# Performance work log

Hardware: AMD Instinct MI355X
Metric: run time of the kernel (lower is better)

Reference implementation:

```python
import jax, jax.numpy as jnp
import numpy as np

N_HEADS = 8
D_KV = 64
NUM_BUCKETS = 32
MAX_DISTANCE = 128


def _relative_position_bucket(relative_position, bidirectional=True,
                              num_buckets=NUM_BUCKETS, max_distance=MAX_DISTANCE):
    # Faithful port of T5Attention._relative_position_bucket (bidirectional path).
    n = -relative_position
    if bidirectional:
        num_buckets //= 2
        ret = (n < 0).astype(jnp.int32) * num_buckets
        n = jnp.abs(n)
    else:
        ret = jnp.zeros_like(n)
        n = jnp.maximum(n, 0)
    max_exact = num_buckets // 2
    is_small = n < max_exact
    val_if_large = max_exact + (
        jnp.log(n.astype(jnp.float32) / max_exact)
        / np.log(max_distance / max_exact)
        * (num_buckets - max_exact)
    ).astype(jnp.int32)
    val_if_large = jnp.minimum(val_if_large, num_buckets - 1)
    return ret + jnp.where(is_small, n, val_if_large)


def setup_inputs() -> dict:
    key = jax.random.key(0)
    ks = jax.random.split(key, 6)
    bs, qlen, d_model = 2, 2048, 512
    inner = N_HEADS * D_KV
    s = 1.0 / np.sqrt(d_model)
    return {
        "input": jax.random.normal(ks[0], (bs, qlen, d_model), jnp.float32),
        "Wq": jax.random.normal(ks[1], (d_model, inner), jnp.float32) * s,
        "Wk": jax.random.normal(ks[2], (d_model, inner), jnp.float32) * s,
        "Wv": jax.random.normal(ks[3], (d_model, inner), jnp.float32) * s,
        "Wo": jax.random.normal(ks[4], (inner, d_model), jnp.float32) * s,
        "rel_bias": jax.random.normal(ks[5], (NUM_BUCKETS, N_HEADS), jnp.float32),
    }


def reference(input, Wq, Wk, Wv, Wo, rel_bias):
    bs, qlen, d_model = input.shape

    def shape(x):  # [b, s, inner] -> [b, h, s, d]
        return x.reshape(bs, qlen, N_HEADS, D_KV).transpose(0, 2, 1, 3)

    q = shape(input @ Wq)
    k = shape(input @ Wk)
    v = shape(input @ Wv)

    # Raw scores (T5: no 1/sqrt(d) scaling)
    scores = jnp.einsum("bhqd,bhkd->bhqk", q, k)

    # Relative position bias: bucket [q, k] -> [h, q, k]
    pos = jnp.arange(qlen)
    rel_pos = pos[None, :] - pos[:, None]  # memory - query
    buckets = _relative_position_bucket(rel_pos, bidirectional=True)
    position_bias = rel_bias[buckets].transpose(2, 0, 1)[None]  # [1, h, q, k]

    scores = scores + position_bias
    weights = jax.nn.softmax(scores.astype(jnp.float32), axis=-1).astype(scores.dtype)

    context = jnp.einsum("bhqk,bhkd->bhqd", weights, v)
    context = context.transpose(0, 2, 1, 3).reshape(bs, qlen, N_HEADS * D_KV)
    return context @ Wo
```

## Files before the change

kernel.cpp:

```cpp
#include <hip/hip_runtime.h>
#include <hip/hip_bf16.h>
#include <cmath>

typedef __bf16 bf16_t;
typedef __bf16 bf16x8 __attribute__((ext_vector_type(8)));
typedef __bf16 bf16x4 __attribute__((ext_vector_type(4)));
typedef float f32x4 __attribute__((ext_vector_type(4)));

#define QLEN 2048
#define DMODEL 512
#define NH 8
#define DKV 64
#define INNER 512
#define LOG2E 1.44269504f
#define THR_LOG2 11.5415603f

__global__ __launch_bounds__(256) void transpose512_split_all(
    const float* __restrict__ W0, const float* __restrict__ W1,
    const float* __restrict__ W2, const float* __restrict__ W3,
    bf16_t* __restrict__ H0, bf16_t* __restrict__ L0,
    bf16_t* __restrict__ H1, bf16_t* __restrict__ L1,
    bf16_t* __restrict__ H2, bf16_t* __restrict__ L2,
    bf16_t* __restrict__ H3, bf16_t* __restrict__ L3) {
  __shared__ float tile[32][33];
  int z = blockIdx.z;
  const float* W = z == 0 ? W0 : z == 1 ? W1 : z == 2 ? W2 : W3;
  bf16_t* Whi    = z == 0 ? H0 : z == 1 ? H1 : z == 2 ? H2 : H3;
  bf16_t* Wlo    = z == 0 ? L0 : z == 1 ? L1 : z == 2 ? L2 : L3;
  int bk = blockIdx.x * 32, bn = blockIdx.y * 32;
  int tx = threadIdx.x, ty = threadIdx.y;
  #pragma unroll
  for (int i = 0; i < 32; i += 8)
    tile[ty + i][tx] = W[(size_t)(bk + ty + i) * DMODEL + bn + tx];
  __syncthreads();
  #pragma unroll
  for (int i = 0; i < 32; i += 8) {
    float v = tile[tx][ty + i];
    bf16_t hb = (bf16_t)v;
    size_t o = (size_t)(bn + ty + i) * DMODEL + bk + tx;
    Whi[o] = hb;
    Wlo[o] = (bf16_t)(v - (float)hb);
  }
}

__device__ __forceinline__ void splitx8(const float4& v0, const float4& v1,
                                        bf16x8& h, bf16x8& l) {
  #pragma unroll
  for (int j = 0; j < 4; ++j) {
    float x = (&v0.x)[j];
    bf16_t hb = (bf16_t)x;
    h[j] = hb; l[j] = (bf16_t)(x - (float)hb);
  }
  #pragma unroll
  for (int j = 0; j < 4; ++j) {
    float x = (&v1.x)[j];
    bf16_t hb = (bf16_t)x;
    h[4 + j] = hb; l[4 + j] = (bf16_t)(x - (float)hb);
  }
}

#define GST 72

__global__ __launch_bounds__(256) void gemm_qkv(const float* __restrict__ X,
                                                const bf16_t* __restrict__ Wqh,
                                                const bf16_t* __restrict__ Wql,
                                                const bf16_t* __restrict__ Wkh,
                                                const bf16_t* __restrict__ Wkl,
                                                const bf16_t* __restrict__ Wvh,
                                                bf16_t* __restrict__ Qh,
                                                bf16_t* __restrict__ Ql,
                                                bf16_t* __restrict__ Kh,
                                                bf16_t* __restrict__ Vt) {
  __shared__ bf16_t sAh[64 * GST];
  __shared__ bf16_t sAl[64 * GST];
  __shared__ bf16_t sBh[128 * GST];
  __shared__ bf16_t sBl[128 * GST];
  const int m0 = blockIdx.x * 64;
  const int y = blockIdx.y;
  const int kind = y >> 2;
  const int n0 = (y & 3) * 128;
  const bf16_t* __restrict__ Bh = kind == 0 ? Wqh : kind == 1 ? Wkh : Wvh;
  const bf16_t* __restrict__ Bl = kind == 0 ? Wql : Wkl;

  const int tid = threadIdx.x;
  const int lane = tid & 63, w = tid >> 6;
  const int wr = (w >> 1) * 32, wc = (w & 1) * 64;
  const int l16 = lane & 15, lg = lane >> 4;

  f32x4 acc[2][4] = {};

  for (int k0 = 0; k0 < DMODEL; k0 += 64) {
    #pragma unroll
    for (int i = 0; i < 2; ++i) {
      int chunk = tid + i * 256;
      int row = chunk >> 3, c8 = (chunk & 7) * 8;
      const float4* src = reinterpret_cast<const float4*>(
          &X[(size_t)(m0 + row) * DMODEL + k0 + c8]);
      bf16x8 h, l;
      splitx8(src[0], src[1], h, l);
      *reinterpret_cast<bf16x8*>(&sAh[row * GST + c8]) = h;
      *reinterpret_cast<bf16x8*>(&sAl[row * GST + c8]) = l;
    }
    #pragma unroll
    for (int i = 0; i < 4; ++i) {
      int chunk = tid + i * 256;
      int row = chunk >> 3, c8 = (chunk & 7) * 8;
      size_t gb = (size_t)(n0 + row) * DMODEL + k0 + c8;
      *reinterpret_cast<bf16x8*>(&sBh[row * GST + c8]) = *reinterpret_cast<const bf16x8*>(&Bh[gb]);
      if (kind < 2)
        *reinterpret_cast<bf16x8*>(&sBl[row * GST + c8]) = *reinterpret_cast<const bf16x8*>(&Bl[gb]);
    }
    __syncthreads();
    #pragma unroll
    for (int ks = 0; ks < 2; ++ks) {
      bf16x8 ah[2], al[2], bh[4], bl[4];
      #pragma unroll
      for (int i = 0; i < 2; ++i) {
        int ro = (wr + i * 16 + l16) * GST + ks * 32 + lg * 8;
        ah[i] = *reinterpret_cast<const bf16x8*>(&sAh[ro]);
        al[i] = *reinterpret_cast<const bf16x8*>(&sAl[ro]);
      }
      #pragma unroll
      for (int j = 0; j < 4; ++j) {
        int ro = (wc + j * 16 + l16) * GST + ks * 32 + lg * 8;
        bh[j] = *reinterpret_cast<const bf16x8*>(&sBh[ro]);
        bl[j] = *reinterpret_cast<const bf16x8*>(&sBl[ro]);
      }
      #pragma unroll
      for (int i = 0; i < 2; ++i)
        #pragma unroll
        for (int j = 0; j < 4; ++j)
          acc[i][j] = __builtin_amdgcn_mfma_f32_16x16x32_bf16(ah[i], bh[j], acc[i][j], 0, 0, 0);
      if (kind < 2) {
        #pragma unroll
        for (int i = 0; i < 2; ++i)
          #pragma unroll
          for (int j = 0; j < 4; ++j) {
            acc[i][j] = __builtin_amdgcn_mfma_f32_16x16x32_bf16(ah[i], bl[j], acc[i][j], 0, 0, 0);
            acc[i][j] = __builtin_amdgcn_mfma_f32_16x16x32_bf16(al[i], bh[j], acc[i][j], 0, 0, 0);
          }
      }
    }
    __syncthreads();
  }

  #pragma unroll
  for (int i = 0; i < 2; ++i)
    #pragma unroll
    for (int j = 0; j < 4; ++j)
      #pragma unroll
      for (int r = 0; r < 4; ++r) {
        int m = m0 + wr + i * 16 + lg * 4 + r;
        int n = n0 + wc + j * 16 + l16;
        float v = acc[i][j][r];
        if (kind == 0) {
          v *= LOG2E;
          bf16_t hb = (bf16_t)v;
          size_t o = (size_t)m * INNER + n;
          Qh[o] = hb;
          Ql[o] = (bf16_t)(v - (float)hb);
        } else if (kind == 1) {
          Kh[(size_t)m * INNER + n] = (bf16_t)v;
        } else {
          int b = m >> 11, s = m & (QLEN - 1);
          Vt[(size_t)(b * INNER + n) * QLEN + s] = (bf16_t)v;
        }
      }
}

__global__ __launch_bounds__(256) void gemm_out(const bf16_t* __restrict__ A,
                                                const bf16_t* __restrict__ Bt,
                                                float* __restrict__ Cf) {
  __shared__ bf16_t sA[64 * GST];
  __shared__ bf16_t sB[64 * GST];
  const int m0 = blockIdx.x * 64, n0 = blockIdx.y * 64;
  const int tid = threadIdx.x;
  const int lane = tid & 63, w = tid >> 6;
  const int wr = (w >> 1) * 32, wc = (w & 1) * 32;
  const int l16 = lane & 15, lg = lane >> 4;

  f32x4 acc[2][2] = {};

  for (int k0 = 0; k0 < DMODEL; k0 += 64) {
    #pragma unroll
    for (int i = 0; i < 2; ++i) {
      int chunk = tid + i * 256;
      int row = chunk >> 3, c8 = (chunk & 7) * 8;
      *reinterpret_cast<bf16x8*>(&sA[row * GST + c8]) =
          *reinterpret_cast<const bf16x8*>(&A[(size_t)(m0 + row) * DMODEL + k0 + c8]);
      *reinterpret_cast<bf16x8*>(&sB[row * GST + c8]) =
          *reinterpret_cast<const bf16x8*>(&Bt[(size_t)(n0 + row) * DMODEL + k0 + c8]);
    }
    __syncthreads();
    #pragma unroll
    for (int ks = 0; ks < 2; ++ks) {
      bf16x8 af[2], bfr[2];
      #pragma unroll
      for (int i = 0; i < 2; ++i)
        af[i] = *reinterpret_cast<const bf16x8*>(&sA[(wr + i * 16 + l16) * GST + ks * 32 + lg * 8]);
      #pragma unroll
      for (int j = 0; j < 2; ++j)
        bfr[j] = *reinterpret_cast<const bf16x8*>(&sB[(wc + j * 16 + l16) * GST + ks * 32 + lg * 8]);
      #pragma unroll
      for (int i = 0; i < 2; ++i)
        #pragma unroll
        for (int j = 0; j < 2; ++j)
          acc[i][j] = __builtin_amdgcn_mfma_f32_16x16x32_bf16(af[i], bfr[j], acc[i][j], 0, 0, 0);
    }
    __syncthreads();
  }

  #pragma unroll
  for (int i = 0; i < 2; ++i)
    #pragma unroll
    for (int j = 0; j < 2; ++j)
      #pragma unroll
      for (int r = 0; r < 4; ++r) {
        int m = m0 + wr + i * 16 + lg * 4 + r;
        int n = n0 + wc + j * 16 + l16;
        Cf[(size_t)m * DMODEL + n] = acc[i][j][r];
      }
}

__device__ __forceinline__ float redmax16(float v) {
  v = fmaxf(v, __shfl_xor(v, 1));
  v = fmaxf(v, __shfl_xor(v, 2));
  v = fmaxf(v, __shfl_xor(v, 4));
  v = fmaxf(v, __shfl_xor(v, 8));
  return v;
}
__device__ __forceinline__ float redsum16(float v) {
  v += __shfl_xor(v, 1);
  v += __shfl_xor(v, 2);
  v += __shfl_xor(v, 4);
  v += __shfl_xor(v, 8);
  return v;
}
__device__ __forceinline__ int t5_bucket_abs(int n) {
  if (n < 8)  return n;
  if (n < 12) return 8;
  if (n < 16) return 9;
  if (n < 23) return 10;
  if (n < 32) return 11;
  if (n < 46) return 12;
  if (n < 64) return 13;
  if (n < 91) return 14;
  return 15;
}

#define SPS 68
#define SVS 136

__global__ __launch_bounds__(512, 4) void attn_kernel(const bf16_t* __restrict__ Qh,
                                                      const bf16_t* __restrict__ Ql,
                                                      const bf16_t* __restrict__ Kh,
                                                      const bf16_t* __restrict__ Vt,
                                                      const float* __restrict__ relb,
                                                      bf16_t* __restrict__ ctx) {
  __shared__ bf16_t sKh[128 * 72];
  __shared__ bf16_t sV [64 * SVS];
  __shared__ bf16_t sP [2][64 * SPS];
  __shared__ float sM[2][64], sL[2][64];
  __shared__ float sBiasH[32];
  float* sAcc = (float*)&sP[0][0];

  const int id = blockIdx.x;
  const int lin = (id & 7) * 64 + (id >> 3);
  const int qt = lin & 31, h = (lin >> 5) & 7, b = lin >> 8;

  const int tid = threadIdx.x, lane = tid & 63, w = tid >> 6;
  const int l16 = lane & 15, lg = lane >> 4;
  const int q0 = qt * 64;
  const int qg = w & 3, half = w >> 2;
  const int wq = qg * 16;
  const int kh0 = half * 64;

  if (tid < 32) sBiasH[tid] = relb[tid * NH + h] * LOG2E;

  bf16x8 qh[2], ql[2];
  #pragma unroll
  for (int ks = 0; ks < 2; ++ks) {
    size_t o = (size_t)(b * QLEN + q0 + wq + l16) * INNER + h * DKV + ks * 32 + lg * 8;
    qh[ks] = *reinterpret_cast<const bf16x8*>(&Qh[o]);
    ql[ks] = *reinterpret_cast<const bf16x8*>(&Ql[o]);
  }

  f32x4 acc[4] = {};
  float mrow[4], lpart[4];
  #pragma unroll
  for (int r = 0; r < 4; ++r) { mrow[r] = -INFINITY; lpart[r] = 0.f; }

  const int krow = tid >> 3, kc8 = (tid & 7) * 8;
  const int vrow = tid >> 4, vc8 = (tid & 15) * 8;
  const bf16_t* kPtr = Kh + (size_t)(b * QLEN + krow) * INNER + h * DKV + kc8;
  const bf16_t* vPtr = Vt + (size_t)((b * NH + h) * DKV + vrow) * QLEN + vc8;
  const size_t kStep = (size_t)64 * INNER;
  bf16_t* kDst0 = &sKh[krow * 72 + kc8];
  bf16_t* kDst1 = &sKh[(krow + 64) * 72 + kc8];
  bf16_t* vDst0 = &sV[vrow * SVS + vc8];
  bf16_t* vDst1 = &sV[(vrow + 32) * SVS + vc8 + 0];

  bf16x8 rk0, rk1, rv0, rv1;
  rk0 = *reinterpret_cast<const bf16x8*>(kPtr);
  rk1 = *reinterpret_cast<const bf16x8*>(kPtr + kStep);
  rv0 = *reinterpret_cast<const bf16x8*>(vPtr);
  rv1 = *reinterpret_cast<const bf16x8*>(vPtr + (size_t)32 * QLEN);
  *reinterpret_cast<bf16x8*>(kDst0) = rk0;
  *reinterpret_cast<bf16x8*>(kDst1) = rk1;
  *reinterpret_cast<bf16x8*>(vDst0) = rv0;
  *reinterpret_cast<bf16x8*>(vDst1) = rv1;
  __syncthreads();

  const int NT = QLEN / 128;
  for (int kt = 0; kt < NT; ++kt) {
    const int k0 = kt * 128;
    const bool pf = (kt + 1 < NT);
    if (pf) {
      const bf16_t* kp = kPtr + (size_t)(k0 + 128) * INNER;
      const bf16_t* vp = vPtr + k0 + 128;
      rk0 = *reinterpret_cast<const bf16x8*>(kp);
      rk1 = *reinterpret_cast<const bf16x8*>(kp + kStep);
      rv0 = *reinterpret_cast<const bf16x8*>(vp);
      rv1 = *reinterpret_cast<const bf16x8*>(vp + (size_t)32 * QLEN);
    }

    f32x4 s[4] = {};
    __builtin_amdgcn_s_setprio(1);
    #pragma unroll
    for (int ks = 0; ks < 2; ++ks) {
      bf16x8 kf[4];
      #pragma unroll
      for (int ni = 0; ni < 4; ++ni)
        kf[ni] = *reinterpret_cast<const bf16x8*>(
            &sKh[(kh0 + ni * 16 + l16) * 72 + ks * 32 + lg * 8]);
      #pragma unroll
      for (int ni = 0; ni < 4; ++ni) {
        s[ni] = __builtin_amdgcn_mfma_f32_16x16x32_bf16(qh[ks], kf[ni], s[ni], 0, 0, 0);
        s[ni] = __builtin_amdgcn_mfma_f32_16x16x32_bf16(ql[ks], kf[ni], s[ni], 0, 0, 0);
      }
    }
    __builtin_amdgcn_s_setprio(0);

    const int kbase = k0 + kh0;
    const int dmin = q0 - (kbase + 63);
    const int dmax = q0 + 63 - kbase;
    const bool farP = dmin >= 91, farN = dmax <= -91;
    float fbias = 0.f;
    if (farP) fbias = sBiasH[15];
    else if (farN) fbias = sBiasH[31];
    else {
      #pragma unroll
      for (int ni = 0; ni < 4; ++ni) {
        int kcol = kbase + ni * 16 + l16;
        #pragma unroll
        for (int r = 0; r < 4; ++r) {
          int qrow = q0 + wq + lg * 4 + r;
          int d = qrow - kcol;
          int n = d < 0 ? -d : d;
          int bk = t5_bucket_abs(n) + (d < 0 ? 16 : 0);
          s[ni][r] += sBiasH[bk];
        }
      }
    }

    float c[4], tmx[4];
    #pragma unroll
    for (int r = 0; r < 4; ++r) {
      tmx[r] = fmaxf(fmaxf(s[0][r], s[1][r]), fmaxf(s[2][r], s[3][r]));
      c[r] = mrow[r] - fbias;
    }
    float u = fmaxf(fmaxf(tmx[0] - c[0], tmx[1] - c[1]), fmaxf(tmx[2] - c[2], tmx[3] - c[3]));
    if (__any(u > THR_LOG2)) {
      #pragma unroll
      for (int r = 0; r < 4; ++r) {
        float rm = redmax16(tmx[r]) + fbias;
        float mnew = fmaxf(mrow[r], rm);
        float alpha = exp2f(mrow[r] - mnew);
        mrow[r] = mnew;
        c[r] = mnew - fbias;
        lpart[r] *= alpha;
        #pragma unroll
        for (int di = 0; di < 4; ++di) acc[di][r] *= alpha;
      }
    }

    #pragma unroll
    for (int r = 0; r < 4; ++r) {
      float ps = 0.f;
      #pragma unroll
      for (int ni = 0; ni < 4; ++ni) {
        float p = exp2f(s[ni][r] - c[r]);
        ps += p;
        sP[half][(wq + lg * 4 + r) * SPS + ni * 16 + l16] = (bf16_t)p;
      }
      lpart[r] += ps;
    }

    __builtin_amdgcn_s_setprio(1);
    #pragma unroll
    for (int ks = 0; ks < 2; ++ks) {
      bf16x8 pfr, vf[4];
      pfr = *reinterpret_cast<const bf16x8*>(&sP[half][(wq + l16) * SPS + ks * 32 + lg * 8]);
      #pragma unroll
      for (int di = 0; di < 4; ++di)
        vf[di] = *reinterpret_cast<const bf16x8*>(
            &sV[(di * 16 + l16) * SVS + kh0 + ks * 32 + lg * 8]);
      #pragma unroll
      for (int di = 0; di < 4; ++di)
        acc[di] = __builtin_amdgcn_mfma_f32_16x16x32_bf16(pfr, vf[di], acc[di], 0, 0, 0);
    }
    __builtin_amdgcn_s_setprio(0);

    __syncthreads();
    if (pf) {
      *reinterpret_cast<bf16x8*>(kDst0) = rk0;
      *reinterpret_cast<bf16x8*>(kDst1) = rk1;
      *reinterpret_cast<bf16x8*>(vDst0) = rv0;
      *reinterpret_cast<bf16x8*>(vDst1) = rv1;
    }
    __syncthreads();
  }

  float lrow[4];
  #pragma unroll
  for (int r = 0; r < 4; ++r) lrow[r] = redsum16(lpart[r]);

  if (l16 == 0) {
    #pragma unroll
    for (int r = 0; r < 4; ++r) {
      int row = wq + lg * 4 + r;
      sM[half][row] = mrow[r];
      sL[half][row] = lrow[r];
    }
  }
  __syncthreads();

  float eh[4], denom[4];
  #pragma unroll
  for (int r = 0; r < 4; ++r) {
    int row = wq + lg * 4 + r;
    float m0 = sM[0][row], m1 = sM[1][row];
    float l0 = sL[0][row], l1 = sL[1][row];
    float M = fmaxf(m0, m1);
    float e0 = exp2f(m0 - M), e1 = exp2f(m1 - M);
    denom[r] = l0 * e0 + l1 * e1;
    eh[r] = half ? e1 : e0;
  }

  if (half == 1) {
    #pragma unroll
    for (int di = 0; di < 4; ++di)
      #pragma unroll
      for (int r = 0; r < 4; ++r)
        sAcc[(wq + lg * 4 + r) * SPS + di * 16 + l16] = acc[di][r] * eh[r];
  }
  __syncthreads();

  if (half == 0) {
    #pragma unroll
    for (int di = 0; di < 4; ++di)
      #pragma unroll
      for (int r = 0; r < 4; ++r) {
        int row = wq + lg * 4 + r;
        float v = (acc[di][r] * eh[r] + sAcc[row * SPS + di * 16 + l16]) / denom[r];
        ctx[(size_t)(b * QLEN + q0 + row) * INNER + h * DKV + di * 16 + l16] = (bf16_t)v;
      }
  }
}

extern "C" void kernel_launch(void* const* d_in, const int* in_sizes, int n_in,
                              void* d_out, int out_size, void* d_ws, size_t ws_size,
                              hipStream_t stream) {
  const float* X    = (const float*)d_in[0];
  const float* Wq   = (const float*)d_in[1];
  const float* Wk   = (const float*)d_in[2];
  const float* Wv   = (const float*)d_in[3];
  const float* Wo   = (const float*)d_in[4];
  const float* relb = (const float*)d_in[5];
  float* out = (float*)d_out;

  const size_t WSZ = 262144, XSZ = 2097152;
  bf16_t* ws   = (bf16_t*)d_ws;
  bf16_t* Wq_h = ws;              bf16_t* Wq_l = Wq_h + WSZ;
  bf16_t* Wk_h = Wq_l + WSZ;      bf16_t* Wk_l = Wk_h + WSZ;
  bf16_t* Wv_h = Wk_l + WSZ;      bf16_t* Wv_l = Wv_h + WSZ;
  bf16_t* Wo_h = Wv_l + WSZ;      bf16_t* Wo_l = Wo_h + WSZ;
  bf16_t* buf0 = Wo_l + WSZ;      bf16_t* buf1 = buf0 + XSZ;
  bf16_t* Q_h  = buf1 + XSZ;      bf16_t* Q_l  = Q_h + XSZ;
  bf16_t* K_h  = Q_l + XSZ;
  bf16_t* Vt   = buf1;
  bf16_t* ctx  = buf0;

  transpose512_split_all<<<dim3(16, 16, 4), dim3(32, 8), 0, stream>>>(
      Wq, Wk, Wv, Wo, Wq_h, Wq_l, Wk_h, Wk_l, Wv_h, Wv_l, Wo_h, Wo_l);

  gemm_qkv<<<dim3(64, 12), 256, 0, stream>>>(X, Wq_h, Wq_l, Wk_h, Wk_l, Wv_h,
                                             Q_h, Q_l, K_h, Vt);

  attn_kernel<<<dim3(512), 512, 0, stream>>>(Q_h, Q_l, K_h, Vt, relb, ctx);

  gemm_out<<<dim3(64, 8), 256, 0, stream>>>(ctx, Wo_h, out);
}
```

Before: 118.6 us.

## Split QKV projection into separate Q/K split-precision and V plain GEMM kernels

Replaces the combined QKV GEMM, which used 64x128 tiles and branched on Q/K/V kind, with two kernels. One handles Q and K with 64x64 tiles and the three-MFMA hi/lo split. The other is a templated 64x64 GEMM that computes V with a direct fp32->bf16 cast of X and a transposed store, and it also replaces the output projection kernel. Smaller tiles double the block count for Q/K, which improves CU occupancy and removes divergent per-kind work within a grid. The cost is an extra kernel launch and re-reading X for the V projection.

```diff
diff --git a/kernel.cpp b/kernel.cpp
--- a/kernel.cpp
+++ b/kernel.cpp
@@ -58,36 +58,111 @@
     h[4 + j] = hb; l[4 + j] = (bf16_t)(x - (float)hb);
   }
 }
+__device__ __forceinline__ bf16x8 castx8(const float4& v0, const float4& v1) {
+  bf16x8 h;
+  #pragma unroll
+  for (int j = 0; j < 4; ++j) h[j] = (bf16_t)(&v0.x)[j];
+  #pragma unroll
+  for (int j = 0; j < 4; ++j) h[4 + j] = (bf16_t)(&v1.x)[j];
+  return h;
+}
 
 #define GST 72
 
-__global__ __launch_bounds__(256) void gemm_qkv(const float* __restrict__ X,
-                                                const bf16_t* __restrict__ Wqh,
-                                                const bf16_t* __restrict__ Wql,
-                                                const bf16_t* __restrict__ Wkh,
-                                                const bf16_t* __restrict__ Wkl,
-                                                const bf16_t* __restrict__ Wvh,
-                                                bf16_t* __restrict__ Qh,
-                                                bf16_t* __restrict__ Ql,
-                                                bf16_t* __restrict__ Kh,
-                                                bf16_t* __restrict__ Vt) {
+template<int MODE, int AF32>
+__global__ __launch_bounds__(256) void gemm64(const bf16_t* __restrict__ Ab,
+                                              const float* __restrict__ Af,
+                                              const bf16_t* __restrict__ Bt,
+                                              bf16_t* __restrict__ Cb,
+                                              float* __restrict__ Cf) {
+  __shared__ bf16_t sA[64 * GST];
+  __shared__ bf16_t sB[64 * GST];
+  const int m0 = blockIdx.x * 64, n0 = blockIdx.y * 64;
+  const int tid = threadIdx.x;
+  const int lane = tid & 63, w = tid >> 6;
+  const int wr = (w >> 1) * 32, wc = (w & 1) * 32;
+  const int l16 = lane & 15, lg = lane >> 4;
+
+  f32x4 acc[2][2] = {};
+
+  for (int k0 = 0; k0 < DMODEL; k0 += 64) {
+    #pragma unroll
+    for (int i = 0; i < 2; ++i) {
+      int chunk = tid + i * 256;
+      int row = chunk >> 3, c8 = (chunk & 7) * 8;
+      if (AF32) {
+        const float4* src = reinterpret_cast<const float4*>(
+            &Af[(size_t)(m0 + row) * DMODEL + k0 + c8]);
+        *reinterpret_cast<bf16x8*>(&sA[row * GST + c8]) = castx8(src[0], src[1]);
+      } else {
+        *reinterpret_cast<bf16x8*>(&sA[row * GST + c8]) =
+            *reinterpret_cast<const bf16x8*>(&Ab[(size_t)(m0 + row) * DMODEL + k0 + c8]);
+      }
+      *reinterpret_cast<bf16x8*>(&sB[row * GST + c8]) =
+          *reinterpret_cast<const bf16x8*>(&Bt[(size_t)(n0 + row) * DMODEL + k0 + c8]);
+    }
+    __syncthreads();
+    #pragma unroll
+    for (int ks = 0; ks < 2; ++ks) {
+      bf16x8 af[2], bfr[2];
+      #pragma unroll
+      for (int i = 0; i < 2; ++i)
+        af[i] = *reinterpret_cast<const bf16x8*>(&sA[(wr + i * 16 + l16) * GST + ks * 32 + lg * 8]);
+      #pragma unroll
+      for (int j = 0; j < 2; ++j)
+        bfr[j] = *reinterpret_cast<const bf16x8*>(&sB[(wc + j * 16 + l16) * GST + ks * 32 + lg * 8]);
+      #pragma unroll
+      for (int i = 0; i < 2; ++i)
+        #pragma unroll
+        for (int j = 0; j < 2; ++j)
+          acc[i][j] = __builtin_amdgcn_mfma_f32_16x16x32_bf16(af[i], bfr[j], acc[i][j], 0, 0, 0);
+    }
+    __syncthreads();
+  }
+
+  #pragma unroll
+  for (int i = 0; i < 2; ++i)
+    #pragma unroll
+    for (int j = 0; j < 2; ++j)
+      #pragma unroll
+      for (int r = 0; r < 4; ++r) {
+        int m = m0 + wr + i * 16 + lg * 4 + r;
+        int n = n0 + wc + j * 16 + l16;
+        float v = acc[i][j][r];
+        if (MODE == 1) {
+          int b = m >> 11, s = m & (QLEN - 1);
+          Cb[(size_t)(b * INNER + n) * QLEN + s] = (bf16_t)v;
+        } else {
+          Cf[(size_t)m * DMODEL + n] = v;
+        }
+      }
+}
+
+__global__ __launch_bounds__(256) void gemm_qk_split(const float* __restrict__ X,
+                                                     const bf16_t* __restrict__ Bqh,
+                                                     const bf16_t* __restrict__ Bql,
+                                                     const bf16_t* __restrict__ Bkh,
+                                                     const bf16_t* __restrict__ Bkl,
+                                                     bf16_t* __restrict__ Qh,
+                                                     bf16_t* __restrict__ Ql,
+                                                     bf16_t* __restrict__ Kh) {
   __shared__ bf16_t sAh[64 * GST];
   __shared__ bf16_t sAl[64 * GST];
-  __shared__ bf16_t sBh[128 * GST];
-  __shared__ bf16_t sBl[128 * GST];
+  __shared__ bf16_t sBh[64 * GST];
+  __shared__ bf16_t sBl[64 * GST];
   const int m0 = blockIdx.x * 64;
   const int y = blockIdx.y;
-  const int kind = y >> 2;
-  const int n0 = (y & 3) * 128;
-  const bf16_t* __restrict__ Bh = kind == 0 ? Wqh : kind == 1 ? Wkh : Wvh;
-  const bf16_t* __restrict__ Bl = kind == 0 ? Wql : Wkl;
+  const bool isK = y >= 8;
+  const int n0 = (y & 7) * 64;
+  const bf16_t* __restrict__ Bh = isK ? Bkh : Bqh;
+  const bf16_t* __restrict__ Bl = isK ? Bkl : Bql;
 
   const int tid = threadIdx.x;
   const int lane = tid & 63, w = tid >> 6;
-  const int wr = (w >> 1) * 32, wc = (w & 1) * 64;
+  const int wr = (w >> 1) * 32, wc = (w & 1) * 32;
   const int l16 = lane & 15, lg = lane >> 4;
 
-  f32x4 acc[2][4] = {};
+  f32x4 acc[2][2] = {};
 
   for (int k0 = 0; k0 < DMODEL; k0 += 64) {
     #pragma unroll
@@ -100,20 +175,14 @@
       splitx8(src[0], src[1], h, l);
       *reinterpret_cast<bf16x8*>(&sAh[row * GST + c8]) = h;
       *reinterpret_cast<bf16x8*>(&sAl[row * GST + c8]) = l;
-    }
-    #pragma unroll
-    for (int i = 0; i < 4; ++i) {
-      int chunk = tid + i * 256;
-      int row = chunk >> 3, c8 = (chunk & 7) * 8;
       size_t gb = (size_t)(n0 + row) * DMODEL + k0 + c8;
       *reinterpret_cast<bf16x8*>(&sBh[row * GST + c8]) = *reinterpret_cast<const bf16x8*>(&Bh[gb]);
-      if (kind < 2)
-        *reinterpret_cast<bf16x8*>(&sBl[row * GST + c8]) = *reinterpret_cast<const bf16x8*>(&Bl[gb]);
+      *reinterpret_cast<bf16x8*>(&sBl[row * GST + c8]) = *reinterpret_cast<const bf16x8*>(&Bl[gb]);
     }
     __syncthreads();
     #pragma unroll
     for (int ks = 0; ks < 2; ++ks) {
-      bf16x8 ah[2], al[2], bh[4], bl[4];
+      bf16x8 ah[2], al[2], bh[2], bl[2];
       #pragma unroll
       for (int i = 0; i < 2; ++i) {
         int ro = (wr + i * 16 + l16) * GST + ks * 32 + lg * 8;
@@ -121,7 +190,7 @@
         al[i] = *reinterpret_cast<const bf16x8*>(&sAl[ro]);
       }
       #pragma unroll
-      for (int j = 0; j < 4; ++j) {
+      for (int j = 0; j < 2; ++j) {
         int ro = (wc + j * 16 + l16) * GST + ks * 32 + lg * 8;
         bh[j] = *reinterpret_cast<const bf16x8*>(&sBh[ro]);
         bl[j] = *reinterpret_cast<const bf16x8*>(&sBl[ro]);
@@ -129,17 +198,11 @@
       #pragma unroll
       for (int i = 0; i < 2; ++i)
         #pragma unroll
-        for (int j = 0; j < 4; ++j)
+        for (int j = 0; j < 2; ++j) {
           acc[i][j] = __builtin_amdgcn_mfma_f32_16x16x32_bf16(ah[i], bh[j], acc[i][j], 0, 0, 0);
-      if (kind < 2) {
-        #pragma unroll
-        for (int i = 0; i < 2; ++i)
-          #pragma unroll
-          for (int j = 0; j < 4; ++j) {
-            acc[i][j] = __builtin_amdgcn_mfma_f32_16x16x32_bf16(ah[i], bl[j], acc[i][j], 0, 0, 0);
-            acc[i][j] = __builtin_amdgcn_mfma_f32_16x16x32_bf16(al[i], bh[j], acc[i][j], 0, 0, 0);
-          }
-      }
+          acc[i][j] = __builtin_amdgcn_mfma_f32_16x16x32_bf16(ah[i], bl[j], acc[i][j], 0, 0, 0);
+          acc[i][j] = __builtin_amdgcn_mfma_f32_16x16x32_bf16(al[i], bh[j], acc[i][j], 0, 0, 0);
+        }
     }
     __syncthreads();
   }
@@ -147,78 +210,21 @@
   #pragma unroll
   for (int i = 0; i < 2; ++i)
     #pragma unroll
-    for (int j = 0; j < 4; ++j)
+    for (int j = 0; j < 2; ++j)
       #pragma unroll
       for (int r = 0; r < 4; ++r) {
         int m = m0 + wr + i * 16 + lg * 4 + r;
         int n = n0 + wc + j * 16 + l16;
         float v = acc[i][j][r];
-        if (kind == 0) {
+        if (!isK) {
           v *= LOG2E;
           bf16_t hb = (bf16_t)v;
           size_t o = (size_t)m * INNER + n;
           Qh[o] = hb;
           Ql[o] = (bf16_t)(v - (float)hb);
-        } else if (kind == 1) {
+        } else {
           Kh[(size_t)m * INNER + n] = (bf16_t)v;
-        } else {
-          int b = m >> 11, s = m & (QLEN - 1);
-          Vt[(size_t)(b * INNER + n) * QLEN + s] = (bf16_t)v;
         }
-      }
-}
-
-__global__ __launch_bounds__(256) void gemm_out(const bf16_t* __restrict__ A,
-                                                const bf16_t* __restrict__ Bt,
-                                                float* __restrict__ Cf) {
-  __shared__ bf16_t sA[64 * GST];
-  __shared__ bf16_t sB[64 * GST];
-  const int m0 = blockIdx.x * 64, n0 = blockIdx.y * 64;
-  const int tid = threadIdx.x;
-  const int lane = tid & 63, w = tid >> 6;
-  const int wr = (w >> 1) * 32, wc = (w & 1) * 32;
-  const int l16 = lane & 15, lg = lane >> 4;
-
-  f32x4 acc[2][2] = {};
-
-  for (int k0 = 0; k0 < DMODEL; k0 += 64) {
-    #pragma unroll
-    for (int i = 0; i < 2; ++i) {
-      int chunk = tid + i * 256;
-      int row = chunk >> 3, c8 = (chunk & 7) * 8;
-      *reinterpret_cast<bf16x8*>(&sA[row * GST + c8]) =
-          *reinterpret_cast<const bf16x8*>(&A[(size_t)(m0 + row) * DMODEL + k0 + c8]);
-      *reinterpret_cast<bf16x8*>(&sB[row * GST + c8]) =
-          *reinterpret_cast<const bf16x8*>(&Bt[(size_t)(n0 + row) * DMODEL + k0 + c8]);
-    }
-    __syncthreads();
-    #pragma unroll
-    for (int ks = 0; ks < 2; ++ks) {
-      bf16x8 af[2], bfr[2];
-      #pragma unroll
-      for (int i = 0; i < 2; ++i)
-        af[i] = *reinterpret_cast<const bf16x8*>(&sA[(wr + i * 16 + l16) * GST + ks * 32 + lg * 8]);
-      #pragma unroll
-      for (int j = 0; j < 2; ++j)
-        bfr[j] = *reinterpret_cast<const bf16x8*>(&sB[(wc + j * 16 + l16) * GST + ks * 32 + lg * 8]);
-      #pragma unroll
-      for (int i = 0; i < 2; ++i)
-        #pragma unroll
-        for (int j = 0; j < 2; ++j)
-          acc[i][j] = __builtin_amdgcn_mfma_f32_16x16x32_bf16(af[i], bfr[j], acc[i][j], 0, 0, 0);
-    }
-    __syncthreads();
-  }
-
-  #pragma unroll
-  for (int i = 0; i < 2; ++i)
-    #pragma unroll
-    for (int j = 0; j < 2; ++j)
-      #pragma unroll
-      for (int r = 0; r < 4; ++r) {
-        int m = m0 + wr + i * 16 + lg * 4 + r;
-        int n = n0 + wc + j * 16 + l16;
-        Cf[(size_t)m * DMODEL + n] = acc[i][j][r];
       }
 }
 
@@ -298,7 +304,7 @@
   bf16_t* kDst0 = &sKh[krow * 72 + kc8];
   bf16_t* kDst1 = &sKh[(krow + 64) * 72 + kc8];
   bf16_t* vDst0 = &sV[vrow * SVS + vc8];
-  bf16_t* vDst1 = &sV[(vrow + 32) * SVS + vc8 + 0];
+  bf16_t* vDst1 = &sV[(vrow + 32) * SVS + vc8];
 
   bf16x8 rk0, rk1, rv0, rv1;
   rk0 = *reinterpret_cast<const bf16x8*>(kPtr);
@@ -494,10 +500,11 @@
   transpose512_split_all<<<dim3(16, 16, 4), dim3(32, 8), 0, stream>>>(
       Wq, Wk, Wv, Wo, Wq_h, Wq_l, Wk_h, Wk_l, Wv_h, Wv_l, Wo_h, Wo_l);
 
-  gemm_qkv<<<dim3(64, 12), 256, 0, stream>>>(X, Wq_h, Wq_l, Wk_h, Wk_l, Wv_h,
-                                             Q_h, Q_l, K_h, Vt);
+  gemm_qk_split<<<dim3(64, 16), 256, 0, stream>>>(X, Wq_h, Wq_l, Wk_h, Wk_l,
+                                                  Q_h, Q_l, K_h);
+  gemm64<1, 1><<<dim3(64, 8), 256, 0, stream>>>(nullptr, X, Wv_h, Vt, nullptr);
 
   attn_kernel<<<dim3(512), 512, 0, stream>>>(Q_h, Q_l, K_h, Vt, relb, ctx);
 
-  gemm_out<<<dim3(64, 8), 256, 0, stream>>>(ctx, Wo_h, out);
-}
+  gemm64<2, 0><<<dim3(64, 8), 256, 0, stream>>>(ctx, nullptr, Wo_h, nullptr, out);
+}
```

New measurement: 105.7 us. -10.9%, faster.
